# Kernel optimization log

Measured on AMD Instinct MI355X. Metric: run time of the kernel, lower is better.

## Reference

```python
import jax, jax.numpy as jnp
import numpy as np

K_V = 0.5
G_OFF = 0.001
G_ON = 0.005
N_IN = 4096
N_OUT = 4096
BATCH = 8192


def setup_inputs() -> dict:
    key = jax.random.key(0)
    k1, k2, k3 = jax.random.split(key, 3)
    x = jax.random.normal(k1, (BATCH, N_IN), dtype=jnp.float32)
    # RandomNormal(stddev=1/sqrt(neurons_in)) initializer
    w = jax.random.normal(k2, (N_IN, N_OUT), dtype=jnp.float32) / np.sqrt(N_IN)
    # bias initialized to 0 in the module; use small noise so it is non-degenerate
    b = jax.random.normal(k3, (N_OUT,), dtype=jnp.float32) * 0.01
    return {"x": x, "w": w, "b": b}


def reference(x, w, b):
    # combine_weights: fold bias as an extra input row, x gets a ones column
    weights = jnp.concatenate([w, b[None, :]], axis=0)            # (n_in+1, n_out)
    ones = jnp.ones((x.shape[0], 1), dtype=x.dtype)
    voltages = K_V * jnp.concatenate([x, ones], axis=1)           # (B, n_in+1)

    # weights_to_conductances, 'lowest' mapping rule (differential pair)
    max_weight = jnp.max(jnp.abs(weights))
    k_cond = (G_ON - G_OFF) / max_weight
    g_eff = k_cond * weights
    g_pos = G_OFF + jnp.maximum(g_eff, 0.0)                       # even columns
    g_neg = G_OFF - jnp.minimum(g_eff, 0.0)                       # odd columns
    # interleave pos/neg -> (n_in+1, 2*n_out)
    conductances = jnp.stack([g_pos, g_neg], axis=-1).reshape(weights.shape[0], -1)

    # crossbar currents: scaled GEMM
    currents = voltages @ conductances                            # (B, 2*n_out)

    # differential current subtraction + rescale back to weight domain
    total_currents = currents[:, 0::2] - currents[:, 1::2]        # (B, n_out)
    y_disturbed = total_currents / (K_V * k_cond)
    return y_disturbed
```

## Files before the change

### kernel.cpp

```cpp
#include <hip/hip_runtime.h>
#include <cstdint>

typedef unsigned short u16;
typedef __attribute__((ext_vector_type(8))) __bf16 bf16x8;
typedef __attribute__((ext_vector_type(4))) float f32x4;

#define M_DIM 8192
#define N_DIM 4096
#define K_DIM 4096

#define CVT_X_BLOCKS 16384
#define CVT_W_BLOCKS 2048

__device__ __forceinline__ u16 f2bf(float f) {
    union { float f; uint32_t u; } v; v.f = f;
    uint32_t u = v.u;
    u += 0x7FFFu + ((u >> 16) & 1u);
    return (u16)(u >> 16);
}

__global__ __launch_bounds__(256) void cvt_kernel(const float* __restrict__ x,
                                                  const float* __restrict__ w,
                                                  u16* __restrict__ xb,
                                                  u16* __restrict__ wt) {
    const int t = threadIdx.x;
    if (blockIdx.x < CVT_X_BLOCKS) {
        size_t i = ((size_t)blockIdx.x * 256 + t) * 8;
        const float4* p = (const float4*)(x + i);
        float4 v0 = p[0], v1 = p[1];
        uint32_t o0 = (uint32_t)f2bf(v0.x) | ((uint32_t)f2bf(v0.y) << 16);
        uint32_t o1 = (uint32_t)f2bf(v0.z) | ((uint32_t)f2bf(v0.w) << 16);
        uint32_t o2 = (uint32_t)f2bf(v1.x) | ((uint32_t)f2bf(v1.y) << 16);
        uint32_t o3 = (uint32_t)f2bf(v1.z) | ((uint32_t)f2bf(v1.w) << 16);
        uint4 o; o.x = o0; o.y = o1; o.z = o2; o.w = o3;
        *(uint4*)(xb + i) = o;
    } else {
        const int bid = blockIdx.x - CVT_X_BLOCKS;
        const int k0 = (bid & 63) * 64;
        const int n0 = (bid >> 6) * 128;
        const int wv = t >> 6, l = t & 63;
        const int a  = l & 7;
        const int g  = l >> 3;
        const int kk = k0 + a * 8;
        const int nn = n0 + wv * 32 + g * 4;

        uint32_t b[8][4];
#pragma unroll
        for (int j = 0; j < 8; ++j) {
            float4 v = *(const float4*)&w[(size_t)(kk + j) * N_DIM + nn];
            b[j][0] = f2bf(v.x); b[j][1] = f2bf(v.y);
            b[j][2] = f2bf(v.z); b[j][3] = f2bf(v.w);
        }
#pragma unroll
        for (int i = 0; i < 4; ++i) {
            uint4 o;
            o.x = b[0][i] | (b[1][i] << 16);
            o.y = b[2][i] | (b[3][i] << 16);
            o.z = b[4][i] | (b[5][i] << 16);
            o.w = b[6][i] | (b[7][i] << 16);
            *(uint4*)&wt[(size_t)(nn + i) * K_DIM + kk] = o;
        }
    }
}

typedef const uint32_t __attribute__((address_space(1)))* gp_t;
typedef uint32_t __attribute__((address_space(3)))* lp_t;

#define BK 32
#define NTILES (K_DIM / BK)
#define TN_TILES (N_DIM / 256)
#define NWG ((M_DIM / 256) * TN_TILES)

__global__ __launch_bounds__(512, 2) void gemm_kernel(const u16* __restrict__ A,
                                                      const u16* __restrict__ Bt,
                                                      const float* __restrict__ bias,
                                                      float* __restrict__ C) {
    __shared__ u16 As[2][256][32];
    __shared__ u16 Bs[2][256][32];

    const int t    = threadIdx.x;
    const int lane = t & 63;
    const int l16  = lane & 15;
    const int quad = lane >> 4;
    const int wave = t >> 6;
    const int wr   = wave >> 2;
    const int wc   = wave & 3;

    const int bid = blockIdx.x;
    const int wg  = (bid & 7) * (NWG >> 3) + (bid >> 3);
    const int bm  = (wg / TN_TILES) * 256;
    const int bn  = (wg % TN_TILES) * 256;

    const int rC0 = t >> 2;
    const int rC1 = rC0 + 128;
    const int kcS = ((t & 3) ^ ((rC0 >> 1) & 3)) * 8;
    const u16* a0 = A  + (size_t)(bm + rC0) * K_DIM + kcS;
    const u16* a1 = A  + (size_t)(bm + rC1) * K_DIM + kcS;
    const u16* b0 = Bt + (size_t)(bn + rC0) * K_DIM + kcS;
    const u16* b1 = Bt + (size_t)(bn + rC1) * K_DIM + kcS;

    const int sw8 = (quad ^ ((l16 >> 1) & 3)) * 8;

    f32x4 acc[8][4] = {};
    bf16x8 af[8], bf[4];

#define STAGE_A(buf, kk) do {                                                                   \
        __builtin_amdgcn_global_load_lds((gp_t)(a0 + (kk)), (lp_t)&As[buf][rC0][(t & 3) * 8], 16, 0, 0); \
        __builtin_amdgcn_global_load_lds((gp_t)(a1 + (kk)), (lp_t)&As[buf][rC1][(t & 3) * 8], 16, 0, 0); \
    } while (0)
#define STAGE_B(buf, kk) do {                                                                   \
        __builtin_amdgcn_global_load_lds((gp_t)(b0 + (kk)), (lp_t)&Bs[buf][rC0][(t & 3) * 8], 16, 0, 0); \
        __builtin_amdgcn_global_load_lds((gp_t)(b1 + (kk)), (lp_t)&Bs[buf][rC1][(t & 3) * 8], 16, 0, 0); \
    } while (0)

    STAGE_A(0, 0); STAGE_B(0, 0);

#pragma unroll 2
    for (int tt = 0; tt < NTILES; ++tt) {
        const int nb = tt & 1;
        const int pb = nb ^ 1;
        const int kn = (tt + 1 < NTILES) ? (tt + 1) * BK : 0;

        STAGE_A(pb, kn); STAGE_B(pb, kn);
        asm volatile("s_waitcnt vmcnt(4)" ::: "memory");
        __builtin_amdgcn_s_barrier();

#pragma unroll
        for (int i = 0; i < 8; ++i)
            af[i] = *(const bf16x8*)&As[nb][wr * 128 + i * 16 + l16][sw8];
#pragma unroll
        for (int j = 0; j < 4; ++j)
            bf[j] = *(const bf16x8*)&Bs[nb][wc * 64 + j * 16 + l16][sw8];

        __builtin_amdgcn_s_setprio(1);
#pragma unroll
        for (int i = 0; i < 8; ++i)
#pragma unroll
            for (int j = 0; j < 4; ++j)
                acc[i][j] = __builtin_amdgcn_mfma_f32_16x16x32_bf16(af[i], bf[j], acc[i][j], 0, 0, 0);
        __builtin_amdgcn_s_setprio(0);

        __builtin_amdgcn_s_barrier();
    }

#pragma unroll
    for (int j = 0; j < 4; ++j) {
        const int col = bn + wc * 64 + j * 16 + l16;
        const float bv = bias[col];
#pragma unroll
        for (int i = 0; i < 8; ++i) {
            const int row = bm + wr * 128 + i * 16 + quad * 4;
#pragma unroll
            for (int r = 0; r < 4; ++r)
                C[(size_t)(row + r) * N_DIM + col] = acc[i][j][r] + bv;
        }
    }
#undef STAGE_A
#undef STAGE_B
}

extern "C" void kernel_launch(void* const* d_in, const int* in_sizes, int n_in,
                              void* d_out, int out_size, void* d_ws, size_t ws_size,
                              hipStream_t stream) {
    const float* x = (const float*)d_in[0];
    const float* w = (const float*)d_in[1];
    const float* b = (const float*)d_in[2];
    float* out = (float*)d_out;

    u16* xb = (u16*)d_ws;
    u16* wt = xb + (size_t)M_DIM * K_DIM;

    cvt_kernel<<<CVT_X_BLOCKS + CVT_W_BLOCKS, 256, 0, stream>>>(x, w, xb, wt);
    gemm_kernel<<<dim3(NWG), 512, 0, stream>>>(xb, wt, b, out);
}
```

Before: 553.8 us.

## Fuse fp32-to-bf16 conversion of activations into GEMM tile loading

The separate pass that converted x to bf16 in workspace is removed. The GEMM now loads fp32 x tiles into registers, converts them to bf16 after the MFMA block, and writes them into a padded LDS buffer for the next iteration. Only the weight transpose-convert remains as a pre-pass. This saves a full read and write of the activation matrix. In exchange, the GEMM reads twice as many A bytes from global memory, does conversion ALU work and register staging inside the main loop, and the A load latency is no longer hidden by the async global-to-LDS path.

```diff
diff --git a/kernel.cpp b/kernel.cpp
--- a/kernel.cpp
+++ b/kernel.cpp
@@ -9,57 +9,42 @@
 #define N_DIM 4096
 #define K_DIM 4096
 
-#define CVT_X_BLOCKS 16384
 #define CVT_W_BLOCKS 2048
 
-__device__ __forceinline__ u16 f2bf(float f) {
+__device__ __forceinline__ uint32_t f2bf(float f) {
     union { float f; uint32_t u; } v; v.f = f;
     uint32_t u = v.u;
     u += 0x7FFFu + ((u >> 16) & 1u);
-    return (u16)(u >> 16);
+    return u >> 16;
 }
 
-__global__ __launch_bounds__(256) void cvt_kernel(const float* __restrict__ x,
-                                                  const float* __restrict__ w,
-                                                  u16* __restrict__ xb,
+__global__ __launch_bounds__(256) void cvt_kernel(const float* __restrict__ w,
                                                   u16* __restrict__ wt) {
     const int t = threadIdx.x;
-    if (blockIdx.x < CVT_X_BLOCKS) {
-        size_t i = ((size_t)blockIdx.x * 256 + t) * 8;
-        const float4* p = (const float4*)(x + i);
-        float4 v0 = p[0], v1 = p[1];
-        uint32_t o0 = (uint32_t)f2bf(v0.x) | ((uint32_t)f2bf(v0.y) << 16);
-        uint32_t o1 = (uint32_t)f2bf(v0.z) | ((uint32_t)f2bf(v0.w) << 16);
-        uint32_t o2 = (uint32_t)f2bf(v1.x) | ((uint32_t)f2bf(v1.y) << 16);
-        uint32_t o3 = (uint32_t)f2bf(v1.z) | ((uint32_t)f2bf(v1.w) << 16);
-        uint4 o; o.x = o0; o.y = o1; o.z = o2; o.w = o3;
-        *(uint4*)(xb + i) = o;
-    } else {
-        const int bid = blockIdx.x - CVT_X_BLOCKS;
-        const int k0 = (bid & 63) * 64;
-        const int n0 = (bid >> 6) * 128;
-        const int wv = t >> 6, l = t & 63;
-        const int a  = l & 7;
-        const int g  = l >> 3;
-        const int kk = k0 + a * 8;
-        const int nn = n0 + wv * 32 + g * 4;
+    const int bid = blockIdx.x;
+    const int k0 = (bid & 63) * 64;
+    const int n0 = (bid >> 6) * 128;
+    const int wv = t >> 6, l = t & 63;
+    const int a  = l & 7;
+    const int g  = l >> 3;
+    const int kk = k0 + a * 8;
+    const int nn = n0 + wv * 32 + g * 4;
 
-        uint32_t b[8][4];
+    uint32_t b[8][4];
 #pragma unroll
-        for (int j = 0; j < 8; ++j) {
-            float4 v = *(const float4*)&w[(size_t)(kk + j) * N_DIM + nn];
-            b[j][0] = f2bf(v.x); b[j][1] = f2bf(v.y);
-            b[j][2] = f2bf(v.z); b[j][3] = f2bf(v.w);
-        }
+    for (int j = 0; j < 8; ++j) {
+        float4 v = *(const float4*)&w[(size_t)(kk + j) * N_DIM + nn];
+        b[j][0] = f2bf(v.x); b[j][1] = f2bf(v.y);
+        b[j][2] = f2bf(v.z); b[j][3] = f2bf(v.w);
+    }
 #pragma unroll
-        for (int i = 0; i < 4; ++i) {
-            uint4 o;
-            o.x = b[0][i] | (b[1][i] << 16);
-            o.y = b[2][i] | (b[3][i] << 16);
-            o.z = b[4][i] | (b[5][i] << 16);
-            o.w = b[6][i] | (b[7][i] << 16);
-            *(uint4*)&wt[(size_t)(nn + i) * K_DIM + kk] = o;
-        }
+    for (int i = 0; i < 4; ++i) {
+        uint4 o;
+        o.x = b[0][i] | (b[1][i] << 16);
+        o.y = b[2][i] | (b[3][i] << 16);
+        o.z = b[4][i] | (b[5][i] << 16);
+        o.w = b[6][i] | (b[7][i] << 16);
+        *(uint4*)&wt[(size_t)(nn + i) * K_DIM + kk] = o;
     }
 }
 
@@ -71,11 +56,11 @@
 #define TN_TILES (N_DIM / 256)
 #define NWG ((M_DIM / 256) * TN_TILES)
 
-__global__ __launch_bounds__(512, 2) void gemm_kernel(const u16* __restrict__ A,
+__global__ __launch_bounds__(512, 2) void gemm_kernel(const float* __restrict__ X,
                                                       const u16* __restrict__ Bt,
                                                       const float* __restrict__ bias,
                                                       float* __restrict__ C) {
-    __shared__ u16 As[2][256][32];
+    __shared__ u16 As[2][256][40];
     __shared__ u16 Bs[2][256][32];
 
     const int t    = threadIdx.x;
@@ -91,11 +76,13 @@
     const int bm  = (wg / TN_TILES) * 256;
     const int bn  = (wg % TN_TILES) * 256;
 
-    const int rC0 = t >> 2;
-    const int rC1 = rC0 + 128;
-    const int kcS = ((t & 3) ^ ((rC0 >> 1) & 3)) * 8;
-    const u16* a0 = A  + (size_t)(bm + rC0) * K_DIM + kcS;
-    const u16* a1 = A  + (size_t)(bm + rC1) * K_DIM + kcS;
+    const int rC0  = t >> 2;
+    const int rC1  = rC0 + 128;
+    const int qs   = t & 3;
+    const int slot = qs ^ ((rC0 >> 1) & 3);
+    const float* xa0 = X + (size_t)(bm + rC0) * K_DIM + qs * 8;
+    const float* xa1 = X + (size_t)(bm + rC1) * K_DIM + qs * 8;
+    const int kcS = slot * 8;
     const u16* b0 = Bt + (size_t)(bn + rC0) * K_DIM + kcS;
     const u16* b1 = Bt + (size_t)(bn + rC1) * K_DIM + kcS;
 
@@ -104,16 +91,28 @@
     f32x4 acc[8][4] = {};
     bf16x8 af[8], bf[4];
 
-#define STAGE_A(buf, kk) do {                                                                   \
-        __builtin_amdgcn_global_load_lds((gp_t)(a0 + (kk)), (lp_t)&As[buf][rC0][(t & 3) * 8], 16, 0, 0); \
-        __builtin_amdgcn_global_load_lds((gp_t)(a1 + (kk)), (lp_t)&As[buf][rC1][(t & 3) * 8], 16, 0, 0); \
+#define STAGE_B(buf, kk) do {                                                                   \
+        __builtin_amdgcn_global_load_lds((gp_t)(b0 + (kk)), (lp_t)&Bs[buf][rC0][qs * 8], 16, 0, 0); \
+        __builtin_amdgcn_global_load_lds((gp_t)(b1 + (kk)), (lp_t)&Bs[buf][rC1][qs * 8], 16, 0, 0); \
     } while (0)
-#define STAGE_B(buf, kk) do {                                                                   \
-        __builtin_amdgcn_global_load_lds((gp_t)(b0 + (kk)), (lp_t)&Bs[buf][rC0][(t & 3) * 8], 16, 0, 0); \
-        __builtin_amdgcn_global_load_lds((gp_t)(b1 + (kk)), (lp_t)&Bs[buf][rC1][(t & 3) * 8], 16, 0, 0); \
+#define CVT_WRITE_A(buf)  do {                                                \
+        uint4 o0, o1;                                                         \
+        o0.x = f2bf(a00.x) | (f2bf(a00.y) << 16);                             \
+        o0.y = f2bf(a00.z) | (f2bf(a00.w) << 16);                             \
+        o0.z = f2bf(a01.x) | (f2bf(a01.y) << 16);                             \
+        o0.w = f2bf(a01.z) | (f2bf(a01.w) << 16);                             \
+        o1.x = f2bf(a10.x) | (f2bf(a10.y) << 16);                             \
+        o1.y = f2bf(a10.z) | (f2bf(a10.w) << 16);                             \
+        o1.z = f2bf(a11.x) | (f2bf(a11.y) << 16);                             \
+        o1.w = f2bf(a11.z) | (f2bf(a11.w) << 16);                             \
+        *(uint4*)&As[buf][rC0][slot * 8] = o0;                                \
+        *(uint4*)&As[buf][rC1][slot * 8] = o1;                                \
     } while (0)
 
-    STAGE_A(0, 0); STAGE_B(0, 0);
+    float4 a00 = *(const float4*)(xa0 + 0), a01 = *(const float4*)(xa0 + 4);
+    float4 a10 = *(const float4*)(xa1 + 0), a11 = *(const float4*)(xa1 + 4);
+    STAGE_B(0, 0);
+    CVT_WRITE_A(0);
 
 #pragma unroll 2
     for (int tt = 0; tt < NTILES; ++tt) {
@@ -121,8 +120,12 @@
         const int pb = nb ^ 1;
         const int kn = (tt + 1 < NTILES) ? (tt + 1) * BK : 0;
 
-        STAGE_A(pb, kn); STAGE_B(pb, kn);
-        asm volatile("s_waitcnt vmcnt(4)" ::: "memory");
+        a00 = *(const float4*)(xa0 + kn); a01 = *(const float4*)(xa0 + kn + 4);
+        a10 = *(const float4*)(xa1 + kn); a11 = *(const float4*)(xa1 + kn + 4);
+        STAGE_B(pb, kn);
+
+        asm volatile("s_waitcnt vmcnt(6)" ::: "memory");
+        asm volatile("s_waitcnt lgkmcnt(0)" ::: "memory");
         __builtin_amdgcn_s_barrier();
 
 #pragma unroll
@@ -140,6 +143,8 @@
                 acc[i][j] = __builtin_amdgcn_mfma_f32_16x16x32_bf16(af[i], bf[j], acc[i][j], 0, 0, 0);
         __builtin_amdgcn_s_setprio(0);
 
+        CVT_WRITE_A(pb);
+
         __builtin_amdgcn_s_barrier();
     }
 
@@ -155,8 +160,8 @@
                 C[(size_t)(row + r) * N_DIM + col] = acc[i][j][r] + bv;
         }
     }
-#undef STAGE_A
 #undef STAGE_B
+#undef CVT_WRITE_A
 }
 
 extern "C" void kernel_launch(void* const* d_in, const int* in_sizes, int n_in,
@@ -167,9 +172,8 @@
     const float* b = (const float*)d_in[2];
     float* out = (float*)d_out;
 
-    u16* xb = (u16*)d_ws;
-    u16* wt = xb + (size_t)M_DIM * K_DIM;
+    u16* wt = (u16*)d_ws;
 
-    cvt_kernel<<<CVT_X_BLOCKS + CVT_W_BLOCKS, 256, 0, stream>>>(x, w, xb, wt);
-    gemm_kernel<<<dim3(NWG), 512, 0, stream>>>(xb, wt, b, out);
+    cvt_kernel<<<CVT_W_BLOCKS, 256, 0, stream>>>(w, wt);
+    gemm_kernel<<<dim3(NWG), 512, 0, stream>>>(x, wt, b, out);
 }
```

Measured after the change: 657.1 us. +18.6%, slower.
